# Optimization experiments

Measured on AMD Instinct MI355X. Metric: run time of the kernel, lower is better.

Reference implementation:

```python
import jax, jax.numpy as jnp
import numpy as np

N_EMBD = 1024
COND = 1024
N_HEAD = 16
B, N, NTOK = 4, 2048, 2048


def setup_inputs() -> dict:
    key = jax.random.key(0)
    ks = jax.random.split(key, 10)
    s = 0.02
    return {
        "x": jax.random.normal(ks[0], (B, N, N_EMBD), jnp.float32),
        "encoder_output": jax.random.normal(ks[1], (B, NTOK, COND), jnp.float32),
        "Wq": jax.random.normal(ks[2], (N_EMBD, N_EMBD), jnp.float32) * s,
        "bq": jnp.zeros((N_EMBD,), jnp.float32),
        "Wk": jax.random.normal(ks[3], (N_EMBD, COND), jnp.float32) * s,
        "bk": jnp.zeros((N_EMBD,), jnp.float32),
        "Wv": jax.random.normal(ks[4], (N_EMBD, COND), jnp.float32) * s,
        "bv": jnp.zeros((N_EMBD,), jnp.float32),
        "Wp": jax.random.normal(ks[5], (N_EMBD, N_EMBD), jnp.float32) * s,
        "bp": jnp.zeros((N_EMBD,), jnp.float32),
    }


def reference(x, encoder_output, Wq, bq, Wk, bk, Wv, bv, Wp, bp):
    Bx, Nx, C = x.shape
    H = N_HEAD
    D = C // H
    # projections (torch Linear: y = x @ W^T + b)
    q = (x @ Wq.T + bq).reshape(Bx, Nx, H, D)               # b n h d
    k = (encoder_output @ Wk.T + bk).reshape(Bx, -1, H, D)  # b t h d
    v = (encoder_output @ Wv.T + bv).reshape(Bx, -1, H, D)
    scale = 1.0 / jnp.sqrt(jnp.asarray(D, x.dtype))
    att = jnp.einsum("bnhd,bthd->bhnt", q, k) * scale
    att = jax.nn.softmax(att, axis=-1)
    y = jnp.einsum("bhnt,bthd->bnhd", att, v).reshape(Bx, Nx, C)
    y = y @ Wp.T + bp  # dropout is identity at inference (p effectively 0)
    return y
```

## Files before the change

kernel.cpp:

```cpp
#include <hip/hip_runtime.h>

typedef short bf16x8 __attribute__((ext_vector_type(8)));
typedef float f32x4 __attribute__((ext_vector_type(4)));
typedef unsigned int u32x2 __attribute__((ext_vector_type(2)));

#define AS1 __attribute__((address_space(1)))
#define AS3 __attribute__((address_space(3)))

__device__ __forceinline__ void gld16(void* lds, const void* g) {
  __builtin_amdgcn_global_load_lds((const AS1 unsigned int*)g,
                                   (AS3 unsigned int*)lds, 16, 0, 0);
}

__device__ __forceinline__ unsigned short f2bf(float f) {
  union { float f; unsigned int u; } c; c.f = f;
  return (unsigned short)((c.u + 0x7FFFu + ((c.u >> 16) & 1u)) >> 16);
}

__device__ __forceinline__ unsigned int cvtpk(float lo, float hi) {
  unsigned int r;
  asm("v_cvt_pk_bf16_f32 %0, %1, %2" : "=v"(r) : "v"(lo), "v"(hi));
  return r;
}

__global__ void cvt_kernel(const float4* __restrict__ in, ushort4* __restrict__ out, int n4) {
  int i = blockIdx.x * blockDim.x + threadIdx.x;
  int stride = gridDim.x * blockDim.x;
  for (; i < n4; i += stride) {
    float4 v = in[i];
    ushort4 o;
    o.x = f2bf(v.x); o.y = f2bf(v.y); o.z = f2bf(v.z); o.w = f2bf(v.w);
    out[i] = o;
  }
}

__global__ void cvtw_kernel(const float4* w0, const float4* w1,
                            const float4* w2, const float4* w3,
                            ushort4* o0, ushort4* o1, ushort4* o2, ushort4* o3,
                            int n4) {
  const float4* in; ushort4* out;
  switch (blockIdx.y) {
    case 0: in = w0; out = o0; break;
    case 1: in = w1; out = o1; break;
    case 2: in = w2; out = o2; break;
    default: in = w3; out = o3; break;
  }
  int i = blockIdx.x * blockDim.x + threadIdx.x;
  int stride = gridDim.x * blockDim.x;
  for (; i < n4; i += stride) {
    float4 v = in[i];
    ushort4 o;
    o.x = f2bf(v.x); o.y = f2bf(v.y); o.z = f2bf(v.z); o.w = f2bf(v.w);
    out[i] = o;
  }
}

__global__ __launch_bounds__(256) void gemm_bt_kernel(
    const unsigned short* __restrict__ A,
    const unsigned short* W,
    const float* bias,
    unsigned short* outB,
    float* outF,
    const unsigned short* W2,
    const float* bias2,
    unsigned short* outB2,
    int M, int N, int K, float scale, int splitX)
{
  __shared__ alignas(16) unsigned short As[2][4 * 128 * 8];
  __shared__ alignas(16) unsigned short Bs[2][4 * 128 * 8];

  int bx = blockIdx.x;
  if (bx >= splitX) { W = W2; bias = bias2; outB = outB2; bx -= splitX; }

  const int tid = threadIdx.x;
  const int lane = tid & 63;
  const int w = tid >> 6;
  const int wr = (w >> 1) * 64;
  const int wc = (w & 1) * 64;
  const int lrow = lane & 15;
  const int lk = lane >> 4;
  const long m0 = (long)blockIdx.y * 128;
  const long n0 = (long)bx * 128;

  f32x4 acc[4][4] = {};

  const int c0 = tid, c1 = tid + 256;
  const unsigned short* Ag0 = A + (m0 + (c0 & 127)) * (long)K + (c0 >> 7) * 8;
  const unsigned short* Ag1 = A + (m0 + (c1 & 127)) * (long)K + (c1 >> 7) * 8;
  const unsigned short* Wg0 = W + (n0 + (c0 & 127)) * (long)K + (c0 >> 7) * 8;
  const unsigned short* Wg1 = W + (n0 + (c1 & 127)) * (long)K + (c1 >> 7) * 8;

  const int arow = wr + lrow;
  const int brow = wc + lrow;
  const int nt = K >> 5;

  gld16(As[0] + c0 * 8, Ag0);
  gld16(As[0] + c1 * 8, Ag1);
  gld16(Bs[0] + c0 * 8, Wg0);
  gld16(Bs[0] + c1 * 8, Wg1);

  int cur = 0;
  for (int t = 0; t < nt; ++t) {
    __syncthreads();
    if (t + 1 < nt) {
      const int kt = (t + 1) * 32;
      gld16(As[cur ^ 1] + c0 * 8, Ag0 + kt);
      gld16(As[cur ^ 1] + c1 * 8, Ag1 + kt);
      gld16(Bs[cur ^ 1] + c0 * 8, Wg0 + kt);
      gld16(Bs[cur ^ 1] + c1 * 8, Wg1 + kt);
    }
    const unsigned short* as = As[cur];
    const unsigned short* bs = Bs[cur];
    bf16x8 af[4], bfr[4];
#pragma unroll
    for (int i = 0; i < 4; ++i)
      af[i] = *(const bf16x8*)(as + (lk * 128 + arow + i * 16) * 8);
#pragma unroll
    for (int j = 0; j < 4; ++j)
      bfr[j] = *(const bf16x8*)(bs + (lk * 128 + brow + j * 16) * 8);
#pragma unroll
    for (int i = 0; i < 4; ++i)
#pragma unroll
      for (int j = 0; j < 4; ++j)
        acc[i][j] = __builtin_amdgcn_mfma_f32_16x16x32_bf16(af[i], bfr[j], acc[i][j], 0, 0, 0);
    cur ^= 1;
  }

#pragma unroll
  for (int j = 0; j < 4; ++j) {
    const long col = n0 + wc + j * 16 + lrow;
    const float bv = bias[col];
#pragma unroll
    for (int i = 0; i < 4; ++i) {
#pragma unroll
      for (int r = 0; r < 4; ++r) {
        const long row = m0 + wr + i * 16 + lk * 4 + r;
        float v = (acc[i][j][r] + bv) * scale;
        if (outF) outF[row * (long)N + col] = v;
        else      outB[row * (long)N + col] = f2bf(v);
      }
    }
  }
}

__device__ __forceinline__ int vt_off(int d, int t) {
  const int c = (d ^ (d >> 3)) & 7;
  return d * 64 + (((((t >> 3) ^ c) & 7) << 3) | (t & 7));
}

__global__ __launch_bounds__(256) void attn_kernel(
    const unsigned short* __restrict__ Q,
    const unsigned short* __restrict__ K,
    const unsigned short* __restrict__ V,
    unsigned short* __restrict__ Y)
{
  __shared__ alignas(16) unsigned short Ks[2][8 * 64 * 8];
  __shared__ alignas(16) unsigned short Vt[2][64 * 64];
  __shared__ alignas(16) unsigned short Ps[64 * 72];

  const int tid = threadIdx.x;
  const int lane = tid & 63;
  const int w = tid >> 6;
  const int lrow = lane & 15;
  const int lk = lane >> 4;

  const int id = blockIdx.x;
  const int r8 = id & 7;
  const int s5 = id >> 3;
  const int qt = s5 & 31;
  const int bh = r8 + 8 * (s5 >> 5);
  const int h = bh & 15, b = bh >> 4;
  const long C = 1024, T = 2048, NQ = 2048;

  const unsigned short* Qg = Q + ((long)b * NQ + qt * 64) * C + h * 64;
  const unsigned short* Kg0 = K + (long)b * T * C + h * 64;
  const unsigned short* Vg0 = V + (long)b * T * C + h * 64;

  {
    int c = tid;
    gld16(Ks[0] + c * 8, Kg0 + (long)(c & 63) * C + (c >> 6) * 8);
    c = tid + 256;
    gld16(Ks[0] + c * 8, Kg0 + (long)(c & 63) * C + (c >> 6) * 8);
  }
  bf16x8 qf[2];
#pragma unroll
  for (int kk = 0; kk < 2; ++kk)
    qf[kk] = *(const bf16x8*)(Qg + (long)(w * 16 + lrow) * C + (kk * 4 + lk) * 8);

  const int vrow = tid >> 2;
  const int vseg = (tid & 3) * 16;
  {
    const unsigned short* vgp = Vg0 + (long)vrow * C + vseg;
    bf16x8 v0 = *(const bf16x8*)(vgp);
    bf16x8 v1 = *(const bf16x8*)(vgp + 8);
    unsigned short* vt = Vt[0];
#pragma unroll
    for (int i = 0; i < 8; ++i) vt[vt_off(vseg + i, vrow)] = (unsigned short)v0[i];
#pragma unroll
    for (int i = 0; i < 8; ++i) vt[vt_off(vseg + 8 + i, vrow)] = (unsigned short)v1[i];
  }
  __syncthreads();

  f32x4 o[4] = {};
  float mr = -1e30f, lr = 0.f;
  int cur = 0;

  for (int kt = 0; kt < (int)T; kt += 64) {
    const bool more = (kt + 64 < (int)T);
    bf16x8 nv0, nv1;
    if (more) {
      int c = tid;
      gld16(Ks[cur ^ 1] + c * 8, Kg0 + (long)(kt + 64 + (c & 63)) * C + (c >> 6) * 8);
      c = tid + 256;
      gld16(Ks[cur ^ 1] + c * 8, Kg0 + (long)(kt + 64 + (c & 63)) * C + (c >> 6) * 8);
      const unsigned short* vgn = Vg0 + (long)(kt + 64 + vrow) * C + vseg;
      nv0 = *(const bf16x8*)(vgn);
      nv1 = *(const bf16x8*)(vgn + 8);
    }

    f32x4 s[4] = {};
    __builtin_amdgcn_s_setprio(1);
#pragma unroll
    for (int kk = 0; kk < 2; ++kk) {
#pragma unroll
      for (int j = 0; j < 4; ++j) {
        bf16x8 kf = *(const bf16x8*)(Ks[cur] + ((kk * 4 + lk) * 64 + j * 16 + lrow) * 8);
        s[j] = __builtin_amdgcn_mfma_f32_16x16x32_bf16(kf, qf[kk], s[j], 0, 0, 0);
      }
    }
    __builtin_amdgcn_s_setprio(0);

    float pm;
    {
      float m0 = fmaxf(fmaxf(s[0][0], s[0][1]), fmaxf(s[0][2], s[0][3]));
      float m1 = fmaxf(fmaxf(s[1][0], s[1][1]), fmaxf(s[1][2], s[1][3]));
      float m2 = fmaxf(fmaxf(s[2][0], s[2][1]), fmaxf(s[2][2], s[2][3]));
      float m3 = fmaxf(fmaxf(s[3][0], s[3][1]), fmaxf(s[3][2], s[3][3]));
      pm = fmaxf(fmaxf(m0, m1), fmaxf(m2, m3));
      pm = fmaxf(pm, __shfl_xor(pm, 16));
      pm = fmaxf(pm, __shfl_xor(pm, 32));
    }
    if (__any(pm - mr > 8.0f)) {
      const float mn = fmaxf(mr, pm);
      const float al = __builtin_amdgcn_exp2f(mr - mn);
      mr = mn;
      lr *= al;
#pragma unroll
      for (int j = 0; j < 4; ++j)
#pragma unroll
        for (int r = 0; r < 4; ++r) o[j][r] *= al;
    }
    {
      const int q = w * 16 + lrow;
      float ls = 0.f;
#pragma unroll
      for (int j = 0; j < 4; ++j) {
        float p0 = __builtin_amdgcn_exp2f(s[j][0] - mr);
        float p1 = __builtin_amdgcn_exp2f(s[j][1] - mr);
        float p2 = __builtin_amdgcn_exp2f(s[j][2] - mr);
        float p3 = __builtin_amdgcn_exp2f(s[j][3] - mr);
        ls += (p0 + p1) + (p2 + p3);
        u32x2 pk;
        pk.x = cvtpk(p0, p1);
        pk.y = cvtpk(p2, p3);
        *(u32x2*)(Ps + q * 72 + j * 16 + lk * 4) = pk;
      }
      lr += ls;
    }

    const unsigned short* vt = Vt[cur];
    __builtin_amdgcn_s_setprio(1);
#pragma unroll
    for (int kk = 0; kk < 2; ++kk) {
      bf16x8 pa = *(const bf16x8*)(Ps + (w * 16 + lrow) * 72 + kk * 32 + lk * 8);
#pragma unroll
      for (int j = 0; j < 4; ++j) {
        const int d = j * 16 + lrow;
        const int cs = (d ^ (d >> 3)) & 7;
        bf16x8 vb = *(const bf16x8*)(vt + d * 64 + ((((kk * 4 + lk) ^ cs) & 7) << 3));
        o[j] = __builtin_amdgcn_mfma_f32_16x16x32_bf16(vb, pa, o[j], 0, 0, 0);
      }
    }
    __builtin_amdgcn_s_setprio(0);

    if (more) {
      unsigned short* vtn = Vt[cur ^ 1];
#pragma unroll
      for (int i = 0; i < 8; ++i) vtn[vt_off(vseg + i, vrow)] = (unsigned short)nv0[i];
#pragma unroll
      for (int i = 0; i < 8; ++i) vtn[vt_off(vseg + 8 + i, vrow)] = (unsigned short)nv1[i];
    }
    cur ^= 1;
    __syncthreads();
  }

  unsigned short* Yg = Y + ((long)b * NQ + qt * 64) * C + h * 64;
  float l = lr;
  l += __shfl_xor(l, 16);
  l += __shfl_xor(l, 32);
  const float linv = 1.f / l;
  const int q = w * 16 + lrow;
#pragma unroll
  for (int j = 0; j < 4; ++j) {
    u32x2 pk;
    pk.x = cvtpk(o[j][0] * linv, o[j][1] * linv);
    pk.y = cvtpk(o[j][2] * linv, o[j][3] * linv);
    *(u32x2*)(Yg + (long)q * C + j * 16 + lk * 4) = pk;
  }
}

extern "C" void kernel_launch(void* const* d_in, const int* in_sizes, int n_in,
                              void* d_out, int out_size, void* d_ws, size_t ws_size,
                              hipStream_t stream) {
  (void)in_sizes; (void)n_in; (void)out_size; (void)ws_size;
  const float* x   = (const float*)d_in[0];
  const float* enc = (const float*)d_in[1];
  const float* Wq  = (const float*)d_in[2];
  const float* bq  = (const float*)d_in[3];
  const float* Wk  = (const float*)d_in[4];
  const float* bk  = (const float*)d_in[5];
  const float* Wv  = (const float*)d_in[6];
  const float* bv  = (const float*)d_in[7];
  const float* Wp  = (const float*)d_in[8];
  const float* bp  = (const float*)d_in[9];

  const long M = 4L * 2048;
  const long C = 1024;

  char* ws = (char*)d_ws;
  size_t off = 0;
  auto alloc = [&](size_t bytes) {
    char* p = ws + off;
    off += (bytes + 255) & ~(size_t)255;
    return p;
  };
  unsigned short* Xb  = (unsigned short*)alloc(M * C * 2);
  unsigned short* Eb  = (unsigned short*)alloc(M * C * 2);
  unsigned short* Wqb = (unsigned short*)alloc(C * C * 2);
  unsigned short* Wkb = (unsigned short*)alloc(C * C * 2);
  unsigned short* Wvb = (unsigned short*)alloc(C * C * 2);
  unsigned short* Wpb = (unsigned short*)alloc(C * C * 2);
  unsigned short* Qw  = (unsigned short*)alloc(M * C * 2);
  unsigned short* Kw  = (unsigned short*)alloc(M * C * 2);
  unsigned short* Vw  = (unsigned short*)alloc(M * C * 2);
  unsigned short* Yb  = (unsigned short*)alloc(M * C * 2);

  {
    int n4 = (int)(M * C / 4);
    int blocks = (n4 + 255) / 256; if (blocks > 2048) blocks = 2048;
    cvt_kernel<<<blocks, 256, 0, stream>>>((const float4*)x,   (ushort4*)Xb, n4);
    cvt_kernel<<<blocks, 256, 0, stream>>>((const float4*)enc, (ushort4*)Eb, n4);
    int w4 = (int)(C * C / 4);
    cvtw_kernel<<<dim3(1024, 4), 256, 0, stream>>>(
        (const float4*)Wq, (const float4*)Wk, (const float4*)Wv, (const float4*)Wp,
        (ushort4*)Wqb, (ushort4*)Wkb, (ushort4*)Wvb, (ushort4*)Wpb, w4);
  }

  const float qscale = 0.125f * 1.44269504088896f;
  gemm_bt_kernel<<<dim3(8, 64), 256, 0, stream>>>(
      Xb, Wqb, bq, Qw, nullptr, nullptr, nullptr, nullptr,
      (int)M, (int)C, (int)C, qscale, 999);
  gemm_bt_kernel<<<dim3(16, 64), 256, 0, stream>>>(
      Eb, Wkb, bk, Kw, nullptr, Wvb, bv, Vw,
      (int)M, (int)C, (int)C, 1.0f, 8);

  attn_kernel<<<2048, 256, 0, stream>>>(Qw, Kw, Vw, Yb);

  gemm_bt_kernel<<<dim3(8, 64), 256, 0, stream>>>(
      Yb, Wpb, bp, nullptr, (float*)d_out, nullptr, nullptr, nullptr,
      (int)M, (int)C, (int)C, 1.0f, 999);
}
```

Before: 355.1 us.

## Fuse QKV GEMMs, emit transposed V, and process two query tiles per attention block

Merges the Q and K/V projection GEMMs into one launch, and has the V section write V transposed so attention can stream it into LDS with async global-to-LDS loads instead of a register transpose. The attention block now handles 128 queries (two 64-row tiles) and reuses each K/V tile for both, which halves K/V traffic. The row sum is computed with an MFMA against a ones vector instead of scalar adds and shuffles. The two activation conversion launches are merged into one. The cost is higher register and LDS use per attention block and uncoalesced strided stores for the transposed V.

```diff
diff --git a/kernel.cpp b/kernel.cpp
--- a/kernel.cpp
+++ b/kernel.cpp
@@ -23,7 +23,12 @@
   return r;
 }
 
-__global__ void cvt_kernel(const float4* __restrict__ in, ushort4* __restrict__ out, int n4) {
+__global__ void cvt_kernel(const float4* __restrict__ in0,
+                           const float4* __restrict__ in1,
+                           ushort4* __restrict__ out0,
+                           ushort4* __restrict__ out1, int n4) {
+  const float4* in = blockIdx.y ? in1 : in0;
+  ushort4* out = blockIdx.y ? out1 : out0;
   int i = blockIdx.x * blockDim.x + threadIdx.x;
   int stride = gridDim.x * blockDim.x;
   for (; i < n4; i += stride) {
@@ -55,23 +60,30 @@
   }
 }
 
-__global__ __launch_bounds__(256) void gemm_bt_kernel(
-    const unsigned short* __restrict__ A,
-    const unsigned short* W,
-    const float* bias,
-    unsigned short* outB,
-    float* outF,
-    const unsigned short* W2,
-    const float* bias2,
-    unsigned short* outB2,
-    int M, int N, int K, float scale, int splitX)
+__global__ __launch_bounds__(256) void gemm_qkv_kernel(
+    const unsigned short* __restrict__ Xb,
+    const unsigned short* __restrict__ Eb,
+    const unsigned short* __restrict__ Wqb,
+    const unsigned short* __restrict__ Wkb,
+    const unsigned short* __restrict__ Wvb,
+    const float* __restrict__ bq,
+    const float* __restrict__ bk,
+    const float* __restrict__ bv,
+    unsigned short* __restrict__ Qw,
+    unsigned short* __restrict__ Kw,
+    unsigned short* __restrict__ VTw,
+    float qscale)
 {
   __shared__ alignas(16) unsigned short As[2][4 * 128 * 8];
   __shared__ alignas(16) unsigned short Bs[2][4 * 128 * 8];
 
-  int bx = blockIdx.x;
-  if (bx >= splitX) { W = W2; bias = bias2; outB = outB2; bx -= splitX; }
-
+  const int sec = blockIdx.x >> 3;
+  const int bx = blockIdx.x & 7;
+  const unsigned short* A = (sec == 0) ? Xb : Eb;
+  const unsigned short* W = (sec == 0) ? Wqb : (sec == 1) ? Wkb : Wvb;
+  const float* bias = (sec == 0) ? bq : (sec == 1) ? bk : bv;
+
+  const int K = 1024, N = 1024;
   const int tid = threadIdx.x;
   const int lane = tid & 63;
   const int w = tid >> 6;
@@ -118,6 +130,109 @@
 #pragma unroll
     for (int j = 0; j < 4; ++j)
       bfr[j] = *(const bf16x8*)(bs + (lk * 128 + brow + j * 16) * 8);
+    if (sec != 2) {
+#pragma unroll
+      for (int i = 0; i < 4; ++i)
+#pragma unroll
+        for (int j = 0; j < 4; ++j)
+          acc[i][j] = __builtin_amdgcn_mfma_f32_16x16x32_bf16(af[i], bfr[j], acc[i][j], 0, 0, 0);
+    } else {
+#pragma unroll
+      for (int i = 0; i < 4; ++i)
+#pragma unroll
+        for (int j = 0; j < 4; ++j)
+          acc[i][j] = __builtin_amdgcn_mfma_f32_16x16x32_bf16(bfr[i], af[j], acc[i][j], 0, 0, 0);
+    }
+    cur ^= 1;
+  }
+
+  if (sec != 2) {
+    unsigned short* out = (sec == 0) ? Qw : Kw;
+    const float scale = (sec == 0) ? qscale : 1.0f;
+#pragma unroll
+    for (int j = 0; j < 4; ++j) {
+      const long col = n0 + wc + j * 16 + lrow;
+      const float bv_ = bias[col];
+#pragma unroll
+      for (int i = 0; i < 4; ++i)
+#pragma unroll
+        for (int r = 0; r < 4; ++r) {
+          const long row = m0 + wr + i * 16 + lk * 4 + r;
+          out[row * (long)N + col] = f2bf((acc[i][j][r] + bv_) * scale);
+        }
+    }
+  } else {
+#pragma unroll
+    for (int i = 0; i < 4; ++i)
+#pragma unroll
+      for (int r = 0; r < 4; ++r) {
+        const long feat = n0 + wc + i * 16 + lk * 4 + r;
+        const float bv_ = bias[feat];
+#pragma unroll
+        for (int j = 0; j < 4; ++j) {
+          const long col = m0 + wr + j * 16 + lrow;
+          VTw[feat * 8192 + col] = f2bf(acc[i][j][r] + bv_);
+        }
+      }
+  }
+}
+
+__global__ __launch_bounds__(256) void gemm_bt_kernel(
+    const unsigned short* __restrict__ A,
+    const unsigned short* __restrict__ W,
+    const float* __restrict__ bias,
+    float* __restrict__ outF,
+    int M, int N, int K)
+{
+  __shared__ alignas(16) unsigned short As[2][4 * 128 * 8];
+  __shared__ alignas(16) unsigned short Bs[2][4 * 128 * 8];
+
+  const int tid = threadIdx.x;
+  const int lane = tid & 63;
+  const int w = tid >> 6;
+  const int wr = (w >> 1) * 64;
+  const int wc = (w & 1) * 64;
+  const int lrow = lane & 15;
+  const int lk = lane >> 4;
+  const long m0 = (long)blockIdx.y * 128;
+  const long n0 = (long)blockIdx.x * 128;
+
+  f32x4 acc[4][4] = {};
+
+  const int c0 = tid, c1 = tid + 256;
+  const unsigned short* Ag0 = A + (m0 + (c0 & 127)) * (long)K + (c0 >> 7) * 8;
+  const unsigned short* Ag1 = A + (m0 + (c1 & 127)) * (long)K + (c1 >> 7) * 8;
+  const unsigned short* Wg0 = W + (n0 + (c0 & 127)) * (long)K + (c0 >> 7) * 8;
+  const unsigned short* Wg1 = W + (n0 + (c1 & 127)) * (long)K + (c1 >> 7) * 8;
+
+  const int arow = wr + lrow;
+  const int brow = wc + lrow;
+  const int nt = K >> 5;
+
+  gld16(As[0] + c0 * 8, Ag0);
+  gld16(As[0] + c1 * 8, Ag1);
+  gld16(Bs[0] + c0 * 8, Wg0);
+  gld16(Bs[0] + c1 * 8, Wg1);
+
+  int cur = 0;
+  for (int t = 0; t < nt; ++t) {
+    __syncthreads();
+    if (t + 1 < nt) {
+      const int kt = (t + 1) * 32;
+      gld16(As[cur ^ 1] + c0 * 8, Ag0 + kt);
+      gld16(As[cur ^ 1] + c1 * 8, Ag1 + kt);
+      gld16(Bs[cur ^ 1] + c0 * 8, Wg0 + kt);
+      gld16(Bs[cur ^ 1] + c1 * 8, Wg1 + kt);
+    }
+    const unsigned short* as = As[cur];
+    const unsigned short* bs = Bs[cur];
+    bf16x8 af[4], bfr[4];
+#pragma unroll
+    for (int i = 0; i < 4; ++i)
+      af[i] = *(const bf16x8*)(as + (lk * 128 + arow + i * 16) * 8);
+#pragma unroll
+    for (int j = 0; j < 4; ++j)
+      bfr[j] = *(const bf16x8*)(bs + (lk * 128 + brow + j * 16) * 8);
 #pragma unroll
     for (int i = 0; i < 4; ++i)
 #pragma unroll
@@ -129,34 +244,26 @@
 #pragma unroll
   for (int j = 0; j < 4; ++j) {
     const long col = n0 + wc + j * 16 + lrow;
-    const float bv = bias[col];
-#pragma unroll
-    for (int i = 0; i < 4; ++i) {
+    const float bv_ = bias[col];
+#pragma unroll
+    for (int i = 0; i < 4; ++i)
 #pragma unroll
       for (int r = 0; r < 4; ++r) {
         const long row = m0 + wr + i * 16 + lk * 4 + r;
-        float v = (acc[i][j][r] + bv) * scale;
-        if (outF) outF[row * (long)N + col] = v;
-        else      outB[row * (long)N + col] = f2bf(v);
-      }
-    }
-  }
-}
-
-__device__ __forceinline__ int vt_off(int d, int t) {
-  const int c = (d ^ (d >> 3)) & 7;
-  return d * 64 + (((((t >> 3) ^ c) & 7) << 3) | (t & 7));
+        outF[row * (long)N + col] = acc[i][j][r] + bv_;
+      }
+  }
 }
 
 __global__ __launch_bounds__(256) void attn_kernel(
     const unsigned short* __restrict__ Q,
     const unsigned short* __restrict__ K,
-    const unsigned short* __restrict__ V,
+    const unsigned short* __restrict__ VT,
     unsigned short* __restrict__ Y)
 {
   __shared__ alignas(16) unsigned short Ks[2][8 * 64 * 8];
   __shared__ alignas(16) unsigned short Vt[2][64 * 64];
-  __shared__ alignas(16) unsigned short Ps[64 * 72];
+  __shared__ alignas(16) unsigned short Ps[128 * 72];
 
   const int tid = threadIdx.x;
   const int lane = tid & 63;
@@ -167,145 +274,161 @@
   const int id = blockIdx.x;
   const int r8 = id & 7;
   const int s5 = id >> 3;
-  const int qt = s5 & 31;
-  const int bh = r8 + 8 * (s5 >> 5);
+  const int qt = s5 & 15;
+  const int bh = r8 + 8 * (s5 >> 4);
   const int h = bh & 15, b = bh >> 4;
   const long C = 1024, T = 2048, NQ = 2048;
 
-  const unsigned short* Qg = Q + ((long)b * NQ + qt * 64) * C + h * 64;
+  const unsigned short* Qg = Q + ((long)b * NQ + qt * 128) * C + h * 64;
   const unsigned short* Kg0 = K + (long)b * T * C + h * 64;
-  const unsigned short* Vg0 = V + (long)b * T * C + h * 64;
+  const unsigned short* Vg0 = VT + (long)(h * 64) * 8192 + b * 2048;
 
   {
     int c = tid;
     gld16(Ks[0] + c * 8, Kg0 + (long)(c & 63) * C + (c >> 6) * 8);
     c = tid + 256;
     gld16(Ks[0] + c * 8, Kg0 + (long)(c & 63) * C + (c >> 6) * 8);
-  }
-  bf16x8 qf[2];
-#pragma unroll
-  for (int kk = 0; kk < 2; ++kk)
-    qf[kk] = *(const bf16x8*)(Qg + (long)(w * 16 + lrow) * C + (kk * 4 + lk) * 8);
-
-  const int vrow = tid >> 2;
-  const int vseg = (tid & 3) * 16;
-  {
-    const unsigned short* vgp = Vg0 + (long)vrow * C + vseg;
-    bf16x8 v0 = *(const bf16x8*)(vgp);
-    bf16x8 v1 = *(const bf16x8*)(vgp + 8);
-    unsigned short* vt = Vt[0];
-#pragma unroll
-    for (int i = 0; i < 8; ++i) vt[vt_off(vseg + i, vrow)] = (unsigned short)v0[i];
-#pragma unroll
-    for (int i = 0; i < 8; ++i) vt[vt_off(vseg + 8 + i, vrow)] = (unsigned short)v1[i];
-  }
+    c = tid;
+    gld16(Vt[0] + c * 8, Vg0 + (long)(c >> 3) * 8192 + (((c & 7) ^ ((c >> 3) & 7)) * 8));
+    c = tid + 256;
+    gld16(Vt[0] + c * 8, Vg0 + (long)(c >> 3) * 8192 + (((c & 7) ^ ((c >> 3) & 7)) * 8));
+  }
+  bf16x8 qf[2][2];
+#pragma unroll
+  for (int f = 0; f < 2; ++f)
+#pragma unroll
+    for (int kk = 0; kk < 2; ++kk)
+      qf[f][kk] = *(const bf16x8*)(Qg + (long)(f * 64 + w * 16 + lrow) * C + (kk * 4 + lk) * 8);
+
+  bf16x8 ones;
+#pragma unroll
+  for (int e = 0; e < 8; ++e) ones[e] = (short)0x3F80;
+
   __syncthreads();
 
-  f32x4 o[4] = {};
-  float mr = -1e30f, lr = 0.f;
+  f32x4 oA[4] = {}, oB[4] = {};
+  f32x4 olA = {}, olB = {};
+  float mrA = -1e30f, mrB = -1e30f;
   int cur = 0;
+
+  const int qrow0 = w * 16 + lrow;
 
   for (int kt = 0; kt < (int)T; kt += 64) {
     const bool more = (kt + 64 < (int)T);
-    bf16x8 nv0, nv1;
     if (more) {
       int c = tid;
       gld16(Ks[cur ^ 1] + c * 8, Kg0 + (long)(kt + 64 + (c & 63)) * C + (c >> 6) * 8);
+      gld16(Vt[cur ^ 1] + c * 8,
+            Vg0 + (long)(c >> 3) * 8192 + kt + 64 + (((c & 7) ^ ((c >> 3) & 7)) * 8));
       c = tid + 256;
       gld16(Ks[cur ^ 1] + c * 8, Kg0 + (long)(kt + 64 + (c & 63)) * C + (c >> 6) * 8);
-      const unsigned short* vgn = Vg0 + (long)(kt + 64 + vrow) * C + vseg;
-      nv0 = *(const bf16x8*)(vgn);
-      nv1 = *(const bf16x8*)(vgn + 8);
-    }
-
-    f32x4 s[4] = {};
+      gld16(Vt[cur ^ 1] + c * 8,
+            Vg0 + (long)(c >> 3) * 8192 + kt + 64 + (((c & 7) ^ ((c >> 3) & 7)) * 8));
+    }
+
+    f32x4 sA[4] = {}, sB[4] = {};
     __builtin_amdgcn_s_setprio(1);
 #pragma unroll
     for (int kk = 0; kk < 2; ++kk) {
 #pragma unroll
       for (int j = 0; j < 4; ++j) {
         bf16x8 kf = *(const bf16x8*)(Ks[cur] + ((kk * 4 + lk) * 64 + j * 16 + lrow) * 8);
-        s[j] = __builtin_amdgcn_mfma_f32_16x16x32_bf16(kf, qf[kk], s[j], 0, 0, 0);
+        sA[j] = __builtin_amdgcn_mfma_f32_16x16x32_bf16(kf, qf[0][kk], sA[j], 0, 0, 0);
+        sB[j] = __builtin_amdgcn_mfma_f32_16x16x32_bf16(kf, qf[1][kk], sB[j], 0, 0, 0);
       }
     }
     __builtin_amdgcn_s_setprio(0);
 
-    float pm;
+    float pmA, pmB;
     {
-      float m0 = fmaxf(fmaxf(s[0][0], s[0][1]), fmaxf(s[0][2], s[0][3]));
-      float m1 = fmaxf(fmaxf(s[1][0], s[1][1]), fmaxf(s[1][2], s[1][3]));
-      float m2 = fmaxf(fmaxf(s[2][0], s[2][1]), fmaxf(s[2][2], s[2][3]));
-      float m3 = fmaxf(fmaxf(s[3][0], s[3][1]), fmaxf(s[3][2], s[3][3]));
-      pm = fmaxf(fmaxf(m0, m1), fmaxf(m2, m3));
-      pm = fmaxf(pm, __shfl_xor(pm, 16));
-      pm = fmaxf(pm, __shfl_xor(pm, 32));
-    }
-    if (__any(pm - mr > 8.0f)) {
-      const float mn = fmaxf(mr, pm);
-      const float al = __builtin_amdgcn_exp2f(mr - mn);
-      mr = mn;
-      lr *= al;
-#pragma unroll
-      for (int j = 0; j < 4; ++j)
-#pragma unroll
-        for (int r = 0; r < 4; ++r) o[j][r] *= al;
-    }
-    {
-      const int q = w * 16 + lrow;
-      float ls = 0.f;
-#pragma unroll
-      for (int j = 0; j < 4; ++j) {
-        float p0 = __builtin_amdgcn_exp2f(s[j][0] - mr);
-        float p1 = __builtin_amdgcn_exp2f(s[j][1] - mr);
-        float p2 = __builtin_amdgcn_exp2f(s[j][2] - mr);
-        float p3 = __builtin_amdgcn_exp2f(s[j][3] - mr);
-        ls += (p0 + p1) + (p2 + p3);
-        u32x2 pk;
-        pk.x = cvtpk(p0, p1);
-        pk.y = cvtpk(p2, p3);
-        *(u32x2*)(Ps + q * 72 + j * 16 + lk * 4) = pk;
-      }
-      lr += ls;
+      float a = fmaxf(fmaxf(fmaxf(sA[0][0], sA[0][1]), fmaxf(sA[0][2], sA[0][3])),
+                      fmaxf(fmaxf(sA[1][0], sA[1][1]), fmaxf(sA[1][2], sA[1][3])));
+      float b2 = fmaxf(fmaxf(fmaxf(sA[2][0], sA[2][1]), fmaxf(sA[2][2], sA[2][3])),
+                       fmaxf(fmaxf(sA[3][0], sA[3][1]), fmaxf(sA[3][2], sA[3][3])));
+      pmA = fmaxf(a, b2);
+      pmA = fmaxf(pmA, __shfl_xor(pmA, 16));
+      pmA = fmaxf(pmA, __shfl_xor(pmA, 32));
+      float c2 = fmaxf(fmaxf(fmaxf(sB[0][0], sB[0][1]), fmaxf(sB[0][2], sB[0][3])),
+                       fmaxf(fmaxf(sB[1][0], sB[1][1]), fmaxf(sB[1][2], sB[1][3])));
+      float d2 = fmaxf(fmaxf(fmaxf(sB[2][0], sB[2][1]), fmaxf(sB[2][2], sB[2][3])),
+                       fmaxf(fmaxf(sB[3][0], sB[3][1]), fmaxf(sB[3][2], sB[3][3])));
+      pmB = fmaxf(c2, d2);
+      pmB = fmaxf(pmB, __shfl_xor(pmB, 16));
+      pmB = fmaxf(pmB, __shfl_xor(pmB, 32));
+    }
+    if (__any(fmaxf(pmA - mrA, pmB - mrB) > 8.0f)) {
+      {
+        const float mn = fmaxf(mrA, pmA);
+        const float al = __builtin_amdgcn_exp2f(mrA - mn);
+        mrA = mn; olA *= al;
+#pragma unroll
+        for (int j = 0; j < 4; ++j) oA[j] *= al;
+      }
+      {
+        const float mn = fmaxf(mrB, pmB);
+        const float al = __builtin_amdgcn_exp2f(mrB - mn);
+        mrB = mn; olB *= al;
+#pragma unroll
+        for (int j = 0; j < 4; ++j) oB[j] *= al;
+      }
+    }
+#pragma unroll
+    for (int j = 0; j < 4; ++j) {
+      float p0 = __builtin_amdgcn_exp2f(sA[j][0] - mrA);
+      float p1 = __builtin_amdgcn_exp2f(sA[j][1] - mrA);
+      float p2 = __builtin_amdgcn_exp2f(sA[j][2] - mrA);
+      float p3 = __builtin_amdgcn_exp2f(sA[j][3] - mrA);
+      u32x2 pk;
+      pk.x = cvtpk(p0, p1);
+      pk.y = cvtpk(p2, p3);
+      *(u32x2*)(Ps + qrow0 * 72 + j * 16 + lk * 4) = pk;
+    }
+#pragma unroll
+    for (int j = 0; j < 4; ++j) {
+      float p0 = __builtin_amdgcn_exp2f(sB[j][0] - mrB);
+      float p1 = __builtin_amdgcn_exp2f(sB[j][1] - mrB);
+      float p2 = __builtin_amdgcn_exp2f(sB[j][2] - mrB);
+      float p3 = __builtin_amdgcn_exp2f(sB[j][3] - mrB);
+      u32x2 pk;
+      pk.x = cvtpk(p0, p1);
+      pk.y = cvtpk(p2, p3);
+      *(u32x2*)(Ps + (64 + qrow0) * 72 + j * 16 + lk * 4) = pk;
     }
 
     const unsigned short* vt = Vt[cur];
     __builtin_amdgcn_s_setprio(1);
 #pragma unroll
     for (int kk = 0; kk < 2; ++kk) {
-      bf16x8 pa = *(const bf16x8*)(Ps + (w * 16 + lrow) * 72 + kk * 32 + lk * 8);
+      bf16x8 pa0 = *(const bf16x8*)(Ps + qrow0 * 72 + kk * 32 + lk * 8);
+      bf16x8 pa1 = *(const bf16x8*)(Ps + (64 + qrow0) * 72 + kk * 32 + lk * 8);
+      olA = __builtin_amdgcn_mfma_f32_16x16x32_bf16(ones, pa0, olA, 0, 0, 0);
+      olB = __builtin_amdgcn_mfma_f32_16x16x32_bf16(ones, pa1, olB, 0, 0, 0);
 #pragma unroll
       for (int j = 0; j < 4; ++j) {
         const int d = j * 16 + lrow;
-        const int cs = (d ^ (d >> 3)) & 7;
-        bf16x8 vb = *(const bf16x8*)(vt + d * 64 + ((((kk * 4 + lk) ^ cs) & 7) << 3));
-        o[j] = __builtin_amdgcn_mfma_f32_16x16x32_bf16(vb, pa, o[j], 0, 0, 0);
+        bf16x8 vb = *(const bf16x8*)(vt + d * 64 + ((((kk * 4 + lk) ^ (d & 7)) & 7) << 3));
+        oA[j] = __builtin_amdgcn_mfma_f32_16x16x32_bf16(vb, pa0, oA[j], 0, 0, 0);
+        oB[j] = __builtin_amdgcn_mfma_f32_16x16x32_bf16(vb, pa1, oB[j], 0, 0, 0);
       }
     }
     __builtin_amdgcn_s_setprio(0);
 
-    if (more) {
-      unsigned short* vtn = Vt[cur ^ 1];
-#pragma unroll
-      for (int i = 0; i < 8; ++i) vtn[vt_off(vseg + i, vrow)] = (unsigned short)nv0[i];
-#pragma unroll
-      for (int i = 0; i < 8; ++i) vtn[vt_off(vseg + 8 + i, vrow)] = (unsigned short)nv1[i];
-    }
     cur ^= 1;
     __syncthreads();
   }
 
-  unsigned short* Yg = Y + ((long)b * NQ + qt * 64) * C + h * 64;
-  float l = lr;
-  l += __shfl_xor(l, 16);
-  l += __shfl_xor(l, 32);
-  const float linv = 1.f / l;
-  const int q = w * 16 + lrow;
+  unsigned short* Yg = Y + ((long)b * NQ + qt * 128) * C + h * 64;
+  const float linvA = 1.f / olA[0];
+  const float linvB = 1.f / olB[0];
 #pragma unroll
   for (int j = 0; j < 4; ++j) {
     u32x2 pk;
-    pk.x = cvtpk(o[j][0] * linv, o[j][1] * linv);
-    pk.y = cvtpk(o[j][2] * linv, o[j][3] * linv);
-    *(u32x2*)(Yg + (long)q * C + j * 16 + lk * 4) = pk;
+    pk.x = cvtpk(oA[j][0] * linvA, oA[j][1] * linvA);
+    pk.y = cvtpk(oA[j][2] * linvA, oA[j][3] * linvA);
+    *(u32x2*)(Yg + (long)qrow0 * C + j * 16 + lk * 4) = pk;
+    pk.x = cvtpk(oB[j][0] * linvB, oB[j][1] * linvB);
+    pk.y = cvtpk(oB[j][2] * linvB, oB[j][3] * linvB);
+    *(u32x2*)(Yg + (long)(64 + qrow0) * C + j * 16 + lk * 4) = pk;
   }
 }
 
@@ -342,14 +465,14 @@
   unsigned short* Wpb = (unsigned short*)alloc(C * C * 2);
   unsigned short* Qw  = (unsigned short*)alloc(M * C * 2);
   unsigned short* Kw  = (unsigned short*)alloc(M * C * 2);
-  unsigned short* Vw  = (unsigned short*)alloc(M * C * 2);
+  unsigned short* VTw = (unsigned short*)alloc(M * C * 2);
   unsigned short* Yb  = (unsigned short*)alloc(M * C * 2);
 
   {
     int n4 = (int)(M * C / 4);
     int blocks = (n4 + 255) / 256; if (blocks > 2048) blocks = 2048;
-    cvt_kernel<<<blocks, 256, 0, stream>>>((const float4*)x,   (ushort4*)Xb, n4);
-    cvt_kernel<<<blocks, 256, 0, stream>>>((const float4*)enc, (ushort4*)Eb, n4);
+    cvt_kernel<<<dim3(blocks, 2), 256, 0, stream>>>(
+        (const float4*)x, (const float4*)enc, (ushort4*)Xb, (ushort4*)Eb, n4);
     int w4 = (int)(C * C / 4);
     cvtw_kernel<<<dim3(1024, 4), 256, 0, stream>>>(
         (const float4*)Wq, (const float4*)Wk, (const float4*)Wv, (const float4*)Wp,
@@ -357,16 +480,11 @@
   }
 
   const float qscale = 0.125f * 1.44269504088896f;
+  gemm_qkv_kernel<<<dim3(24, 64), 256, 0, stream>>>(
+      Xb, Eb, Wqb, Wkb, Wvb, bq, bk, bv, Qw, Kw, VTw, qscale);
+
+  attn_kernel<<<1024, 256, 0, stream>>>(Qw, Kw, VTw, Yb);
+
   gemm_bt_kernel<<<dim3(8, 64), 256, 0, stream>>>(
-      Xb, Wqb, bq, Qw, nullptr, nullptr, nullptr, nullptr,
-      (int)M, (int)C, (int)C, qscale, 999);
-  gemm_bt_kernel<<<dim3(16, 64), 256, 0, stream>>>(
-      Eb, Wkb, bk, Kw, nullptr, Wvb, bv, Vw,
-      (int)M, (int)C, (int)C, 1.0f, 8);
-
-  attn_kernel<<<2048, 256, 0, stream>>>(Qw, Kw, Vw, Yb);
-
-  gemm_bt_kernel<<<dim3(8, 64), 256, 0, stream>>>(
-      Yb, Wpb, bp, nullptr, (float*)d_out, nullptr, nullptr, nullptr,
-      (int)M, (int)C, (int)C, 1.0f, 999);
-}
+      Yb, Wpb, bp, (float*)d_out, (int)M, (int)C, (int)C);
+}
```

Result: faster. 298.6 us (-15.9%).
